# Kernel optimization log

Measured on AMD Instinct MI355X. Metric: run time of the kernel, lower is better.

The kernel has to match this reference:

```python
import jax, jax.numpy as jnp
import numpy as np

EMBED_DIM = 1024
NUM_HEADS = 16
HEAD_DIM = EMBED_DIM // NUM_HEADS  # 64
B, H_P, W_P = 4, 48, 48
N = H_P * W_P  # 2304


def setup_inputs() -> dict:
    key = jax.random.key(0)
    ks = jax.random.split(key, 12)
    s = 1.0 / np.sqrt(EMBED_DIM)
    inp = {
        "query": jax.random.normal(ks[0], (B, N, EMBED_DIM), jnp.float32),
        "key": jax.random.normal(ks[1], (B, N, EMBED_DIM), jnp.float32),
        "value": jax.random.normal(ks[2], (B, N, EMBED_DIM), jnp.float32),
        "Wq": jax.random.normal(ks[3], (EMBED_DIM, EMBED_DIM), jnp.float32) * s,
        "bq": jnp.zeros((EMBED_DIM,), jnp.float32),
        "Wk": jax.random.normal(ks[4], (EMBED_DIM, EMBED_DIM), jnp.float32) * s,
        "bk": jnp.zeros((EMBED_DIM,), jnp.float32),
        "Wv": jax.random.normal(ks[5], (EMBED_DIM, EMBED_DIM), jnp.float32) * s,
        "bv": jnp.zeros((EMBED_DIM,), jnp.float32),
        "Wo": jax.random.normal(ks[6], (EMBED_DIM, EMBED_DIM), jnp.float32) * s,
        "bo": jnp.zeros((EMBED_DIM,), jnp.float32),
        "H_patch": H_P,
        "W_patch": W_P,
    }
    return inp


def _rope_2d_cos_sin(h_idx, w_idx, head_dim):
    # 2D RoPE: first half of head_dim encodes the y axis, second half the x axis.
    half = head_dim // 2          # dims per spatial axis (32)
    inv_freq = 1.0 / (10000.0 ** (jnp.arange(0, half, 2, dtype=jnp.float32) / half))  # [half//2]
    fh = h_idx.astype(jnp.float32)[:, None] * inv_freq[None, :]  # [N, half//2]
    fw = w_idx.astype(jnp.float32)[:, None] * inv_freq[None, :]
    emb_h = jnp.concatenate([fh, fh], axis=-1)  # [N, half]
    emb_w = jnp.concatenate([fw, fw], axis=-1)
    emb = jnp.concatenate([emb_h, emb_w], axis=-1)  # [N, head_dim]
    return jnp.cos(emb), jnp.sin(emb)


def _rotate_half_seg(x):
    # rotate_half within a per-axis segment
    h = x.shape[-1] // 2
    return jnp.concatenate([-x[..., h:], x[..., :h]], axis=-1)


def _apply_rotary_2d(x, cos, sin):
    # x: [B, H, N, head_dim]; cos/sin: [N, head_dim]
    half = x.shape[-1] // 2
    c = cos[None, None]
    s = sin[None, None]
    xh, xw = x[..., :half], x[..., half:]
    ch, cw = c[..., :half], c[..., half:]
    sh, sw = s[..., :half], s[..., half:]
    yh = xh * ch + _rotate_half_seg(xh) * sh
    yw = xw * cw + _rotate_half_seg(xw) * sw
    return jnp.concatenate([yh, yw], axis=-1)


def reference(query, key, value, Wq, bq, Wk, bk, Wv, bv, Wo, bo, H_patch, W_patch):
    Bsz, Nn, D = query.shape
    hd = D // NUM_HEADS

    def split_heads(x):
        return x.reshape(Bsz, Nn, NUM_HEADS, hd).transpose(0, 2, 1, 3)  # [B,H,N,hd]

    q = split_heads(query @ Wq.T + bq)
    k = split_heads(key @ Wk.T + bk)
    v = split_heads(value @ Wv.T + bv)

    ys = jnp.arange(H_patch)
    xs = jnp.arange(W_patch)
    yy, xx = jnp.meshgrid(ys, xs, indexing="ij")
    cos, sin = _rope_2d_cos_sin(yy.reshape(-1), xx.reshape(-1), hd)

    q = _apply_rotary_2d(q, cos, sin)
    k = _apply_rotary_2d(k, cos, sin)

    scale = hd ** (-0.5)
    attn = jnp.einsum("bhnd,bhmd->bhnm", q, k) * scale
    attn = jax.nn.softmax(attn, axis=-1)
    out = jnp.einsum("bhnm,bhmd->bhnd", attn, v)
    out = out.transpose(0, 2, 1, 3).reshape(Bsz, Nn, D)
    return out @ Wo.T + bo
```

## Files before the change

kernel.cpp:

```cpp
#include <hip/hip_runtime.h>
#include <cstdint>
#include <cstddef>


typedef __bf16 bf16x8 __attribute__((ext_vector_type(8)));
typedef __bf16 bf16x4 __attribute__((ext_vector_type(4)));
typedef _Float16 f16x4 __attribute__((ext_vector_type(4)));
typedef _Float16 f16x8 __attribute__((ext_vector_type(8)));
typedef float f32x4 __attribute__((ext_vector_type(4)));

constexpr int Bc = 4, Hc = 16, Nc = 2304, Ec = 1024, WPc = 48;
constexpr int BNc = Bc * Nc;

__device__ __forceinline__ f32x4 mfma16(bf16x8 a, bf16x8 b, f32x4 c) {
  return __builtin_amdgcn_mfma_f32_16x16x32_bf16(a, b, c, 0, 0, 0);
}
__device__ __forceinline__ f32x4 mfmah32(f16x8 a, f16x8 b, f32x4 c) {
  return __builtin_amdgcn_mfma_f32_16x16x32_f16(a, b, c, 0, 0, 0);
}

#define GPTR(p) ((const __attribute__((address_space(1))) void*)(p))
#define LPTR(p) ((__attribute__((address_space(3))) void*)(p))

__global__ __launch_bounds__(256) void cvt_all(
    const float* __restrict__ s0, const float* __restrict__ s1,
    const float* __restrict__ s2, const float* __restrict__ s3,
    const float* __restrict__ s4, const float* __restrict__ s5,
    const float* __restrict__ s6, __bf16* __restrict__ d) {
  const size_t EE = (size_t)Ec * Ec, BNE = (size_t)BNc * Ec;
  const size_t g = ((size_t)blockIdx.x * 256 + threadIdx.x) * 8;
  const float* s;
  size_t off;
  if (g < 4 * EE) {
    const size_t a = g >> 20;
    off = g & (EE - 1);
    s = (a == 0) ? s0 : (a == 1) ? s1 : (a == 2) ? s2 : s3;
  } else {
    const size_t h = g - 4 * EE;
    const size_t a = h / BNE;
    off = h - a * BNE;
    s = (a == 0) ? s4 : (a == 1) ? s5 : s6;
  }
  float4 f0 = *(const float4*)(s + off);
  float4 f1 = *(const float4*)(s + off + 4);
  bf16x8 v;
  v[0] = (__bf16)f0.x; v[1] = (__bf16)f0.y; v[2] = (__bf16)f0.z; v[3] = (__bf16)f0.w;
  v[4] = (__bf16)f1.x; v[5] = (__bf16)f1.y; v[6] = (__bf16)f1.z; v[7] = (__bf16)f1.w;
  *(bf16x8*)(d + g) = v;
}

#define GEMM_CORE(APTR, WPTR, KDIM)                                             \
  __shared__ __align__(16) __bf16 As[128 * 32];                                 \
  __shared__ __align__(16) __bf16 Bs[128 * 32];                                 \
  const int t = threadIdx.x;                                                    \
  const int lane = t & 63, wave = t >> 6;                                       \
  const int wm = wave & 1, wn = wave >> 1;                                      \
  const int quad = lane >> 4, l15 = lane & 15;                                  \
  const int rowInC = lane >> 2, colC = (lane & 3) * 8;                          \
  const __bf16* Ab = (APTR) + (size_t)(tm * 128) * (KDIM);                      \
  const __bf16* Wb = (WPTR) + (size_t)(tn * 128) * (KDIM);                      \
  f32x4 zero = {0.f, 0.f, 0.f, 0.f};                                            \
  f32x4 acc[4][4];                                                              \
  for (int i = 0; i < 4; ++i)                                                   \
    for (int j = 0; j < 4; ++j) acc[i][j] = zero;                               \
  for (int kk = 0; kk < (KDIM); kk += 32) {                                     \
    _Pragma("unroll") for (int tch = 0; tch < 2; ++tch) {                       \
      const int ch = wave * 2 + tch;                                            \
      const int row = ch * 16 + rowInC;                                         \
      __builtin_amdgcn_global_load_lds(GPTR(Ab + (size_t)row * (KDIM) + kk + colC), \
                                       LPTR(As + ch * 512), 16, 0, 0);          \
      __builtin_amdgcn_global_load_lds(GPTR(Wb + (size_t)row * (KDIM) + kk + colC), \
                                       LPTR(Bs + ch * 512), 16, 0, 0);          \
    }                                                                           \
    __syncthreads();                                                            \
    bf16x8 af[4], bfg[4];                                                       \
    _Pragma("unroll") for (int i = 0; i < 4; ++i)                               \
        af[i] = *(const bf16x8*)(As + (wm * 64 + i * 16 + l15) * 32 + quad * 8);\
    _Pragma("unroll") for (int j = 0; j < 4; ++j)                               \
        bfg[j] = *(const bf16x8*)(Bs + (wn * 64 + j * 16 + l15) * 32 + quad * 8);\
    _Pragma("unroll") for (int i = 0; i < 4; ++i)                               \
      _Pragma("unroll") for (int j = 0; j < 4; ++j)                             \
        acc[i][j] = mfma16(af[i], bfg[j], acc[i][j]);                           \
    __syncthreads();                                                            \
  }                                                                             \
  const int m0 = tm * 128 + wm * 64;                                            \
  const int nb0 = tn * 128 + wn * 64;

__global__ __launch_bounds__(256) void gemm_qk(const __bf16* __restrict__ qkb,
                                               const __bf16* __restrict__ Wqk,
                                               const float* __restrict__ bq,
                                               const float* __restrict__ bk,
                                               __bf16* __restrict__ Qhp,
                                               __bf16* __restrict__ Khp,
                                               float qscale) {
  const int tn = blockIdx.x & 15;
  const int tm = blockIdx.x >> 4;
  const int proj = tn >> 3;
  const __bf16* Asel = qkb + (size_t)proj * BNc * Ec;
  GEMM_CORE(Asel, Wqk, Ec)

  const int h = (nb0 >> 6) & 15;
  const float* bb = proj ? bk : bq;
  float bj[4];
#pragma unroll
  for (int j = 0; j < 4; ++j) bj[j] = bb[(nb0 + j * 16 + l15) & 1023];
  const float f = exp2f(-(float)l15 * 0.8304820237218406f);
  const int lo3 = l15 & 7, hi8 = l15 >> 3;
#pragma unroll
  for (int i = 0; i < 4; ++i) {
#pragma unroll
    for (int r = 0; r < 4; ++r) {
      const int m = m0 + i * 16 + quad * 4 + r;
      const int b = m / Nc;
      const int ntok = m - b * Nc;
      const int ph = ntok / WPc, pw = ntok - (ntok / WPc) * WPc;
      float sh, ch, sw, cw;
      __sincosf((float)ph * f, &sh, &ch);
      __sincosf((float)pw * f, &sw, &cw);
      const float x0 = acc[i][0][r] + bj[0];
      const float x1 = acc[i][1][r] + bj[1];
      const float x2 = acc[i][2][r] + bj[2];
      const float x3 = acc[i][3][r] + bj[3];
      const float y0 = x0 * ch - x1 * sh;
      const float y1 = x1 * ch + x0 * sh;
      const float y2 = x2 * cw - x3 * sw;
      const float y3 = x3 * cw + x2 * sw;
      if (proj == 0) {
        __bf16* Op = Qhp + ((size_t)(b * Hc + h) * Nc + ntok) * 64;
        Op[l15]      = (__bf16)(y0 * qscale);
        Op[l15 + 16] = (__bf16)(y1 * qscale);
        Op[l15 + 32] = (__bf16)(y2 * qscale);
        Op[l15 + 48] = (__bf16)(y3 * qscale);
      } else {
        const int t64 = ntok & 63;
        const int p64 = (t64 & 35) | ((t64 & 4) << 2) | ((t64 & 24) >> 1);
        __bf16* Kp = Khp + ((size_t)(b * Hc + h) * 36 + (ntok >> 6)) * 4096 +
                     (size_t)((((p64 >> 4) * 2) * 64 + hi8 * 16 + (p64 & 15)) * 8 + lo3);
        Kp[0]   = (__bf16)y0;
        Kp[256] = (__bf16)y1;
        Kp[512] = (__bf16)y2;
        Kp[768] = (__bf16)y3;
      }
    }
  }
}

__global__ __launch_bounds__(256) void gemm_v(const __bf16* __restrict__ A,
                                              const __bf16* __restrict__ Wv,
                                              const float* __restrict__ bv,
                                              _Float16* __restrict__ Vt) {
  const int tn = blockIdx.x & 7;
  const int tm = blockIdx.x >> 3;
  GEMM_CORE(A, Wv, Ec)

  const int h = nb0 >> 6;
#pragma unroll
  for (int i = 0; i < 4; ++i) {
    const int m = m0 + i * 16 + quad * 4;
    const int b = m / Nc;
    const int ntok = m - b * Nc;
    const int t64 = ntok & 63;
    const int c2 = t64 >> 5, qf = (t64 >> 3) & 3, jf0 = t64 & 7;
    const size_t vbase = ((size_t)(b * Hc + h) * 36 + (ntok >> 6)) * 4096;
#pragma unroll
    for (int j = 0; j < 4; ++j) {
      const float bi = bv[nb0 + j * 16 + l15];
      f16x4 v;
#pragma unroll
      for (int r = 0; r < 4; ++r) v[r] = (_Float16)(acc[i][j][r] + bi);
      *(f16x4*)(Vt + vbase +
                (size_t)(((c2 * 4 + j) * 64 + qf * 16 + l15) * 8 + jf0)) = v;
    }
  }
}

__global__ __launch_bounds__(256) void gemm_out(const __bf16* __restrict__ A,
                                                const __bf16* __restrict__ Wo,
                                                const float* __restrict__ bo,
                                                float* __restrict__ C) {
  const int tn = blockIdx.x & 7;
  const int tm = blockIdx.x >> 3;
  GEMM_CORE(A, Wo, Ec)

#pragma unroll
  for (int j = 0; j < 4; ++j) {
    const int n = nb0 + j * 16 + l15;
    const float bi = bo[n];
#pragma unroll
    for (int i = 0; i < 4; ++i) {
      const int m = m0 + i * 16 + quad * 4;
#pragma unroll
      for (int r = 0; r < 4; ++r) C[(size_t)(m + r) * Ec + n] = acc[i][j][r] + bi;
    }
  }
}

constexpr int TQ = 128, TK = 64, NT = Nc / TK;

__global__ __launch_bounds__(256) void attn(const __bf16* __restrict__ Qh,
                                            const __bf16* __restrict__ Kf,
                                            const _Float16* __restrict__ Vf,
                                            __bf16* __restrict__ Om) {
  const int bh = blockIdx.x;
  const int t = threadIdx.x, wave = t >> 6, lane = t & 63;
  const int quad = lane >> 4, l15 = lane & 15;
  const int qbase = blockIdx.y * TQ + wave * 32;

  bf16x8 bq[2][2];
#pragma unroll
  for (int s = 0; s < 2; ++s)
#pragma unroll
    for (int ks = 0; ks < 2; ++ks)
      bq[s][ks] = *(const bf16x8*)(Qh + ((size_t)bh * Nc + qbase + s * 16 + l15) * 64 +
                                   ks * 32 + quad * 8);

  const __bf16* Kb = Kf + (size_t)bh * (NT * 4096) + (size_t)lane * 8;
  const _Float16* Vb = Vf + (size_t)bh * (NT * 4096) + (size_t)lane * 8;

  const f32x4 zero = {0.f, 0.f, 0.f, 0.f};
  f32x4 oacc[2][4] = {{zero, zero, zero, zero}, {zero, zero, zero, zero}};
  f32x4 osum[2] = {zero, zero};
  const f16x8 fones8 = {(_Float16)1.f, (_Float16)1.f, (_Float16)1.f, (_Float16)1.f,
                        (_Float16)1.f, (_Float16)1.f, (_Float16)1.f, (_Float16)1.f};

  for (int kt = 0; kt < NT; ++kt) {
    bf16x8 kf[8];
#pragma unroll
    for (int f = 0; f < 8; ++f)
      kf[f] = *(const bf16x8*)(Kb + (size_t)kt * 4096 + f * 512);
    f16x8 vfr[8];
#pragma unroll
    for (int f = 0; f < 8; ++f)
      vfr[f] = *(const f16x8*)(Vb + (size_t)kt * 4096 + f * 512);

    f32x4 sacc[2][4] = {{zero, zero, zero, zero}, {zero, zero, zero, zero}};
    __builtin_amdgcn_s_setprio(1);
#pragma unroll
    for (int ks = 0; ks < 2; ++ks)
#pragma unroll
      for (int ct = 0; ct < 4; ++ct) {
        sacc[0][ct] = mfma16(kf[ct * 2 + ks], bq[0][ks], sacc[0][ct]);
        sacc[1][ct] = mfma16(kf[ct * 2 + ks], bq[1][ks], sacc[1][ct]);
      }
    __builtin_amdgcn_s_setprio(0);

    f16x8 pf[2][2];
#pragma unroll
    for (int s = 0; s < 2; ++s)
#pragma unroll
      for (int c2 = 0; c2 < 2; ++c2) {
#pragma unroll
        for (int r = 0; r < 4; ++r) {
          pf[s][c2][r]     = (_Float16)exp2f(sacc[s][2 * c2][r]);
          pf[s][c2][4 + r] = (_Float16)exp2f(sacc[s][2 * c2 + 1][r]);
        }
      }

    __builtin_amdgcn_s_setprio(1);
#pragma unroll
    for (int c2 = 0; c2 < 2; ++c2) {
#pragma unroll
      for (int dt = 0; dt < 4; ++dt) {
        oacc[0][dt] = mfmah32(vfr[c2 * 4 + dt], pf[0][c2], oacc[0][dt]);
        oacc[1][dt] = mfmah32(vfr[c2 * 4 + dt], pf[1][c2], oacc[1][dt]);
      }
      osum[0] = mfmah32(fones8, pf[0][c2], osum[0]);
      osum[1] = mfmah32(fones8, pf[1][c2], osum[1]);
    }
    __builtin_amdgcn_s_setprio(0);
  }

  const int b = bh >> 4, h = bh & 15;
#pragma unroll
  for (int s = 0; s < 2; ++s) {
    const float rinv = 1.0f / osum[s][0];
    __bf16* Op = Om + ((size_t)b * Nc + qbase + s * 16 + l15) * Ec + h * 64 + quad * 4;
#pragma unroll
    for (int dt = 0; dt < 4; ++dt) {
      bf16x4 o;
#pragma unroll
      for (int r = 0; r < 4; ++r) o[r] = (__bf16)(oacc[s][dt][r] * rinv);
      *(bf16x4*)(Op + dt * 16) = o;
    }
  }
}

extern "C" void kernel_launch(void* const* d_in, const int* in_sizes, int n_in,
                              void* d_out, int out_size, void* d_ws, size_t ws_size,
                              hipStream_t stream) {
  const float* q  = (const float*)d_in[0];
  const float* k  = (const float*)d_in[1];
  const float* v  = (const float*)d_in[2];
  const float* Wq = (const float*)d_in[3];
  const float* bq = (const float*)d_in[4];
  const float* Wk = (const float*)d_in[5];
  const float* bk = (const float*)d_in[6];
  const float* Wv = (const float*)d_in[7];
  const float* bv = (const float*)d_in[8];
  const float* Wo = (const float*)d_in[9];
  const float* bo = (const float*)d_in[10];
  float* out = (float*)d_out;

  const size_t EE = (size_t)Ec * Ec;
  const size_t BNE = (size_t)BNc * Ec;

  char* w = (char*)d_ws;
  __bf16* Wqkb = (__bf16*)w; w += 2 * EE * 2;
  __bf16* Wvb  = (__bf16*)w; w += EE * 2;
  __bf16* Wob  = (__bf16*)w; w += EE * 2;
  __bf16* qb   = (__bf16*)w; w += BNE * 2;
  __bf16* kb   = (__bf16*)w; w += BNE * 2;
  __bf16* vb   = (__bf16*)w; w += BNE * 2;
  __bf16* Qhp  = (__bf16*)w; w += BNE * 2;
  __bf16* Khp  = (__bf16*)w; w += BNE * 2;
  _Float16* Vtp = (_Float16*)kb;
  __bf16* Omp = qb;

  const dim3 blk(256);
  const dim3 gCvt((4 * EE + 3 * BNE) / 8 / 256);
  const dim3 gQK(16 * (BNc / 128));
  const dim3 gG(8 * (BNc / 128));
  const dim3 gAttn(Bc * Hc, Nc / TQ);

  cvt_all<<<gCvt, blk, 0, stream>>>(Wq, Wk, Wv, Wo, q, k, v, Wqkb);

  const float qscale = 0.125f * 1.44269504088896340736f;

  gemm_qk<<<gQK, blk, 0, stream>>>(qb, Wqkb, bq, bk, Qhp, Khp, qscale);
  gemm_v<<<gG, blk, 0, stream>>>(vb, Wvb, bv, Vtp);
  attn<<<gAttn, blk, 0, stream>>>(Qhp, Khp, Vtp, Omp);
  gemm_out<<<gG, blk, 0, stream>>>(Omp, Wob, bo, out);
}
```

Measured before the change: 448.2 us.

## Double-buffer K/V fragment loads in attention loop and use native exp2

Restructures the attention key loop to software-pipeline global loads of K and V fragments into two register buffers, so the next tile is prefetched while the current one runs through the MFMA and exp steps. It also swaps exp2f for the hardware exp2 builtin when that builtin is available. The prefetch is meant to hide global load latency, and the exp change cuts instructions in the softmax step. In exchange it doubles fragment register use, which can lower occupancy. The loop steps by two, so it assumes NT is even.

```diff
diff --git a/kernel.cpp b/kernel.cpp
--- a/kernel.cpp
+++ b/kernel.cpp
@@ -18,6 +18,12 @@
 __device__ __forceinline__ f32x4 mfmah32(f16x8 a, f16x8 b, f32x4 c) {
   return __builtin_amdgcn_mfma_f32_16x16x32_f16(a, b, c, 0, 0, 0);
 }
+
+#if __has_builtin(__builtin_amdgcn_exp2f)
+#define EXP2F(x) __builtin_amdgcn_exp2f(x)
+#else
+#define EXP2F(x) exp2f(x)
+#endif
 
 #define GPTR(p) ((const __attribute__((address_space(1))) void*)(p))
 #define LPTR(p) ((__attribute__((address_space(3))) void*)(p))
@@ -223,51 +229,54 @@
   const f16x8 fones8 = {(_Float16)1.f, (_Float16)1.f, (_Float16)1.f, (_Float16)1.f,
                         (_Float16)1.f, (_Float16)1.f, (_Float16)1.f, (_Float16)1.f};
 
-  for (int kt = 0; kt < NT; ++kt) {
-    bf16x8 kf[8];
-#pragma unroll
-    for (int f = 0; f < 8; ++f)
-      kf[f] = *(const bf16x8*)(Kb + (size_t)kt * 4096 + f * 512);
-    f16x8 vfr[8];
-#pragma unroll
-    for (int f = 0; f < 8; ++f)
-      vfr[f] = *(const f16x8*)(Vb + (size_t)kt * 4096 + f * 512);
-
-    f32x4 sacc[2][4] = {{zero, zero, zero, zero}, {zero, zero, zero, zero}};
-    __builtin_amdgcn_s_setprio(1);
-#pragma unroll
-    for (int ks = 0; ks < 2; ++ks)
-#pragma unroll
-      for (int ct = 0; ct < 4; ++ct) {
-        sacc[0][ct] = mfma16(kf[ct * 2 + ks], bq[0][ks], sacc[0][ct]);
-        sacc[1][ct] = mfma16(kf[ct * 2 + ks], bq[1][ks], sacc[1][ct]);
-      }
-    __builtin_amdgcn_s_setprio(0);
-
-    f16x8 pf[2][2];
-#pragma unroll
-    for (int s = 0; s < 2; ++s)
-#pragma unroll
-      for (int c2 = 0; c2 < 2; ++c2) {
-#pragma unroll
-        for (int r = 0; r < 4; ++r) {
-          pf[s][c2][r]     = (_Float16)exp2f(sacc[s][2 * c2][r]);
-          pf[s][c2][4 + r] = (_Float16)exp2f(sacc[s][2 * c2 + 1][r]);
-        }
-      }
-
-    __builtin_amdgcn_s_setprio(1);
-#pragma unroll
-    for (int c2 = 0; c2 < 2; ++c2) {
-#pragma unroll
-      for (int dt = 0; dt < 4; ++dt) {
-        oacc[0][dt] = mfmah32(vfr[c2 * 4 + dt], pf[0][c2], oacc[0][dt]);
-        oacc[1][dt] = mfmah32(vfr[c2 * 4 + dt], pf[1][c2], oacc[1][dt]);
-      }
-      osum[0] = mfmah32(fones8, pf[0][c2], osum[0]);
-      osum[1] = mfmah32(fones8, pf[1][c2], osum[1]);
-    }
-    __builtin_amdgcn_s_setprio(0);
+#define LOADKV(KF, VF, KT)                                                      \
+  {                                                                             \
+    _Pragma("unroll") for (int f = 0; f < 8; ++f)                               \
+      KF[f] = *(const bf16x8*)(Kb + (size_t)(KT) * 4096 + f * 512);             \
+    _Pragma("unroll") for (int f = 0; f < 8; ++f)                               \
+      VF[f] = *(const f16x8*)(Vb + (size_t)(KT) * 4096 + f * 512);              \
+  }
+
+#define COMPUTE(KF, VF)                                                         \
+  {                                                                             \
+    f32x4 sacc[2][4] = {{zero, zero, zero, zero}, {zero, zero, zero, zero}};    \
+    __builtin_amdgcn_s_setprio(1);                                              \
+    _Pragma("unroll") for (int ks = 0; ks < 2; ++ks)                            \
+      _Pragma("unroll") for (int ct = 0; ct < 4; ++ct) {                        \
+        sacc[0][ct] = mfma16(KF[ct * 2 + ks], bq[0][ks], sacc[0][ct]);          \
+        sacc[1][ct] = mfma16(KF[ct * 2 + ks], bq[1][ks], sacc[1][ct]);          \
+      }                                                                         \
+    __builtin_amdgcn_s_setprio(0);                                              \
+    f16x8 pf[2][2];                                                             \
+    _Pragma("unroll") for (int s = 0; s < 2; ++s)                               \
+      _Pragma("unroll") for (int c2 = 0; c2 < 2; ++c2) {                        \
+        _Pragma("unroll") for (int r = 0; r < 4; ++r) {                         \
+          pf[s][c2][r]     = (_Float16)EXP2F(sacc[s][2 * c2][r]);               \
+          pf[s][c2][4 + r] = (_Float16)EXP2F(sacc[s][2 * c2 + 1][r]);           \
+        }                                                                       \
+      }                                                                         \
+    __builtin_amdgcn_s_setprio(1);                                              \
+    _Pragma("unroll") for (int c2 = 0; c2 < 2; ++c2) {                          \
+      _Pragma("unroll") for (int dt = 0; dt < 4; ++dt) {                        \
+        oacc[0][dt] = mfmah32(VF[c2 * 4 + dt], pf[0][c2], oacc[0][dt]);         \
+        oacc[1][dt] = mfmah32(VF[c2 * 4 + dt], pf[1][c2], oacc[1][dt]);         \
+      }                                                                         \
+      osum[0] = mfmah32(fones8, pf[0][c2], osum[0]);                            \
+      osum[1] = mfmah32(fones8, pf[1][c2], osum[1]);                            \
+    }                                                                           \
+    __builtin_amdgcn_s_setprio(0);                                              \
+  }
+
+  bf16x8 kfA[8], kfB[8];
+  f16x8 vfA[8], vfB[8];
+  LOADKV(kfA, vfA, 0)
+
+#pragma unroll 1
+  for (int kt = 0; kt < NT; kt += 2) {
+    LOADKV(kfB, vfB, kt + 1)
+    COMPUTE(kfA, vfA)
+    if (kt + 2 < NT) LOADKV(kfA, vfA, kt + 2)
+    COMPUTE(kfB, vfB)
   }
 
   const int b = bh >> 4, h = bh & 15;
@@ -283,6 +292,8 @@
       *(bf16x4*)(Op + dt * 16) = o;
     }
   }
+#undef LOADKV
+#undef COMPUTE
 }
 
 extern "C" void kernel_launch(void* const* d_in, const int* in_sizes, int n_in,
```

Result: faster. 423.2 us (-5.6%).
